# Optimization experiments

Measured on AMD Instinct MI355X. Metric: run time of the kernel, lower is better.

## Reference

```python
import jax, jax.numpy as jnp
import numpy as np
import math

B, S, H, NH, K = 1, 4096, 1024, 16, 32
HD = H // NH


def setup_inputs() -> dict:
    key = jax.random.key(0)
    ks = jax.random.split(key, 8)
    x = jax.random.normal(ks[0], (B, S, H), dtype=jnp.float32)
    # per-query top-K indices; make them causal (idx[q] <= q) so every row has >=1 valid key
    idx_raw = jax.random.randint(ks[1], (S, K), 0, S)
    idx = idx_raw % (jnp.arange(S)[:, None] + 1)
    valid = jnp.ones((S, K), dtype=bool)
    geo_bias = jax.random.normal(ks[2], (NH, S, K), dtype=jnp.float32)
    scale = 1.0 / math.sqrt(H)
    Wq = jax.random.normal(ks[3], (H, H), dtype=jnp.float32) * scale
    Wk = jax.random.normal(ks[4], (H, H), dtype=jnp.float32) * scale
    Wv = jax.random.normal(ks[5], (H, H), dtype=jnp.float32) * scale
    Wo = jax.random.normal(ks[6], (H, H), dtype=jnp.float32) * scale
    bo = jnp.zeros((H,), dtype=jnp.float32)
    return {"x": x, "idx": idx, "valid": valid, "geo_bias": geo_bias,
            "Wq": Wq, "Wk": Wk, "Wv": Wv, "Wo": Wo, "bo": bo}


def reference(x, idx, valid, geo_bias, Wq, Wk, Wv, Wo, bo):
    b, s, h = x.shape
    nh = geo_bias.shape[0]
    hd = h // nh
    kk = idx.shape[1]
    # projections -> [b, nh, s, hd]
    def proj(W):
        return (x @ W).reshape(b, s, nh, hd).transpose(0, 2, 1, 3)
    q, k, v = proj(Wq), proj(Wk), proj(Wv)
    # gather per-query selected keys/values: [b, nh, s, K, hd]
    k_sel = k[:, :, idx]
    v_sel = v[:, :, idx]
    # scores via elementwise mult + reduce over head_dim
    logits = jnp.einsum('bhsd,bhskd->bhsk', q, k_sel) / math.sqrt(hd)
    logits = logits + geo_bias[None]
    mask = valid & (idx <= jnp.arange(s)[:, None])  # [s, K]
    logits = jnp.where(mask[None, None], logits, jnp.float32(-1e30))
    attn = jax.nn.softmax(logits, axis=-1)
    out = jnp.einsum('bhsk,bhskd->bhsd', attn, v_sel)
    out = out.transpose(0, 2, 1, 3).reshape(b, s, h)
    return out @ Wo + bo
```

## Files before the change

kernel.cpp:

```cpp
#include <hip/hip_runtime.h>
#include <hip/hip_bf16.h>
#include <stdint.h>

typedef unsigned short u16;
typedef __attribute__((ext_vector_type(8))) short bf16x8;
typedef __attribute__((ext_vector_type(4))) float f32x4;
typedef __attribute__((ext_vector_type(2))) float f32x2;

typedef const __attribute__((address_space(1))) unsigned int* gptr_t;
typedef __attribute__((address_space(3))) unsigned int* lptr_t;

__device__ __forceinline__ u16 f2bf(float f) {
    unsigned int u;
    __builtin_memcpy(&u, &f, 4);
    u += 0x7FFFu + ((u >> 16) & 1u);
    return (u16)(u >> 16);
}
__device__ __forceinline__ float bflo(unsigned int u) {
    unsigned int x = u << 16; float f; __builtin_memcpy(&f, &x, 4); return f;
}
__device__ __forceinline__ float bfhi(unsigned int u) {
    unsigned int x = u & 0xFFFF0000u; float f; __builtin_memcpy(&f, &x, 4); return f;
}
__device__ __forceinline__ f32x2 upk(unsigned int u) {
    return (f32x2){bflo(u), bfhi(u)};
}

__global__ __launch_bounds__(256) void gemm_qkv(const u16* __restrict__ A,
                                                const u16* __restrict__ Bt,
                                                u16* __restrict__ C,
                                                int M, int N, int K) {
    __shared__ u16 S[4][4096];

    const int t    = threadIdx.x;
    const int lane = t & 63;
    const int wave = t >> 6;
    const int wm   = (wave >> 1) * 64;
    const int wn   = (wave & 1) * 64;
    const int m0   = blockIdx.y * 128;
    const int n0   = blockIdx.x * 128;

    const int r5   = t >> 2;
    const int pc   = t & 3;
    const int lc   = pc ^ ((r5 >> 1) & 3);

    const int quad = lane >> 4;
    const int l16  = lane & 15;
    const int swz  = (l16 >> 1) & 3;

    f32x4 acc[4][4];
#pragma unroll
    for (int i = 0; i < 4; i++)
#pragma unroll
        for (int j = 0; j < 4; j++) acc[i][j] = (f32x4){0.f, 0.f, 0.f, 0.f};

#pragma unroll
    for (int p = 0; p < 2; p++) {
        const u16* ga = A  + (size_t)(m0 + r5 + 64 * p) * K + lc * 8;
        const u16* gb = Bt + (size_t)(n0 + r5 + 64 * p) * K + lc * 8;
        __builtin_amdgcn_global_load_lds((gptr_t)ga, (lptr_t)(&S[0][t * 8 + p * 2048]), 16, 0, 0);
        __builtin_amdgcn_global_load_lds((gptr_t)gb, (lptr_t)(&S[2][t * 8 + p * 2048]), 16, 0, 0);
    }
    __syncthreads();

    const int NT = K >> 5;
    int cur = 0;
    for (int kt = 0; kt < NT; ++kt) {
        if (kt + 1 < NT) {
            const int k0 = (kt + 1) * 32;
#pragma unroll
            for (int p = 0; p < 2; p++) {
                const u16* ga = A  + (size_t)(m0 + r5 + 64 * p) * K + k0 + lc * 8;
                const u16* gb = Bt + (size_t)(n0 + r5 + 64 * p) * K + k0 + lc * 8;
                __builtin_amdgcn_global_load_lds((gptr_t)ga,
                    (lptr_t)(&S[cur ^ 1][t * 8 + p * 2048]), 16, 0, 0);
                __builtin_amdgcn_global_load_lds((gptr_t)gb,
                    (lptr_t)(&S[2 + (cur ^ 1)][t * 8 + p * 2048]), 16, 0, 0);
            }
        }

        bf16x8 af[4], bfg[4];
#pragma unroll
        for (int i = 0; i < 4; i++)
            af[i] = *(const bf16x8*)&S[cur][(wm + i * 16 + l16) * 32 + ((quad ^ swz) * 8)];
#pragma unroll
        for (int j = 0; j < 4; j++)
            bfg[j] = *(const bf16x8*)&S[2 + cur][(wn + j * 16 + l16) * 32 + ((quad ^ swz) * 8)];
#pragma unroll
        for (int i = 0; i < 4; i++)
#pragma unroll
            for (int j = 0; j < 4; j++)
                acc[i][j] = __builtin_amdgcn_mfma_f32_16x16x32_bf16(af[i], bfg[j], acc[i][j], 0, 0, 0);

        __syncthreads();
        cur ^= 1;
    }

    u16* Cs = &S[0][0];
#pragma unroll
    for (int j = 0; j < 4; j++)
#pragma unroll
        for (int i = 0; i < 4; i++)
#pragma unroll
            for (int r = 0; r < 4; r++)
                Cs[(wm + i * 16 + quad * 4 + r) * 128 + wn + j * 16 + l16] = f2bf(acc[i][j][r]);
    __syncthreads();

#pragma unroll
    for (int p = 0; p < 8; p++) {
        const int row = p * 16 + (t >> 4);
        const int c8  = (t & 15) * 8;
        const uint4 v = *(const uint4*)&Cs[row * 128 + c8];
        *(uint4*)&C[(size_t)(m0 + row) * N + n0 + c8] = v;
    }
}

__global__ __launch_bounds__(256) void gemm_o(const u16* __restrict__ A,
                                              const u16* __restrict__ Bt,
                                              float* __restrict__ C,
                                              const float* __restrict__ bias,
                                              int M, int N, int K) {
    __shared__ u16 As[128 * 64];
    __shared__ u16 Bs[64 * 64];

    const int t    = threadIdx.x;
    const int lane = t & 63;
    const int wave = t >> 6;
    const int wm   = (wave >> 1) * 64;
    const int wn   = (wave & 1) * 32;
    const int m0   = blockIdx.y * 128;
    const int n0   = blockIdx.x * 64;

    const int r5   = t >> 3;
    const int pc   = t & 7;
    const int lc   = pc ^ (r5 & 7);

    const int quad = lane >> 4;
    const int l16  = lane & 15;
    const int sw   = l16 & 7;

    f32x4 acc[4][2];
#pragma unroll
    for (int i = 0; i < 4; i++)
#pragma unroll
        for (int j = 0; j < 2; j++) acc[i][j] = (f32x4){0.f, 0.f, 0.f, 0.f};

    for (int k0 = 0; k0 < K; k0 += 64) {
#pragma unroll
        for (int p = 0; p < 4; p++) {
            const u16* ga = A + (size_t)(m0 + r5 + 32 * p) * K + k0 + lc * 8;
            __builtin_amdgcn_global_load_lds((gptr_t)ga, (lptr_t)(&As[t * 8 + p * 2048]), 16, 0, 0);
        }
#pragma unroll
        for (int p = 0; p < 2; p++) {
            const u16* gb = Bt + (size_t)(n0 + r5 + 32 * p) * K + k0 + lc * 8;
            __builtin_amdgcn_global_load_lds((gptr_t)gb, (lptr_t)(&Bs[t * 8 + p * 2048]), 16, 0, 0);
        }
        __syncthreads();

#pragma unroll
        for (int k2 = 0; k2 < 2; k2++) {
            bf16x8 af[4], bfg[2];
#pragma unroll
            for (int i = 0; i < 4; i++)
                af[i] = *(const bf16x8*)&As[(wm + i * 16 + l16) * 64 + ((k2 * 4 + quad) ^ sw) * 8];
#pragma unroll
            for (int j = 0; j < 2; j++)
                bfg[j] = *(const bf16x8*)&Bs[(wn + j * 16 + l16) * 64 + ((k2 * 4 + quad) ^ sw) * 8];
#pragma unroll
            for (int i = 0; i < 4; i++)
#pragma unroll
                for (int j = 0; j < 2; j++)
                    acc[i][j] = __builtin_amdgcn_mfma_f32_16x16x32_bf16(af[i], bfg[j], acc[i][j], 0, 0, 0);
        }
        __syncthreads();
    }

#pragma unroll
    for (int j = 0; j < 2; j++) {
        const int n  = n0 + wn + j * 16 + l16;
        const float bv = bias ? bias[n] : 0.f;
#pragma unroll
        for (int i = 0; i < 4; i++) {
            const int mbase = m0 + wm + i * 16 + quad * 4;
#pragma unroll
            for (int r = 0; r < 4; r++)
                C[(size_t)(mbase + r) * N + n] = acc[i][j][r] + bv;
        }
    }
}

__global__ __launch_bounds__(256) void prep_k(const float* __restrict__ x,
                                              const float* __restrict__ W0,
                                              const float* __restrict__ W1,
                                              const float* __restrict__ W2,
                                              const float* __restrict__ W3,
                                              u16* __restrict__ x_bf,
                                              u16* __restrict__ Dqkv,
                                              u16* __restrict__ Do) {
    const int b = blockIdx.x;
    if (b < 4096) {
        const int i = b * 256 + threadIdx.x;
        const float4 v = ((const float4*)x)[i];
        u16 o[4] = {f2bf(v.x), f2bf(v.y), f2bf(v.z), f2bf(v.w)};
        *(uint64_t*)&x_bf[i * 4] = *(uint64_t*)o;
        return;
    }
    __shared__ u16 tile[32][33];
    const int bb  = b - 4096;
    const int z   = bb >> 10;
    const int t10 = bb & 1023;
    const int c0  = (t10 & 31) * 32;
    const int r0  = (t10 >> 5) * 32;
    const float* src = (z == 0) ? W0 : (z == 1) ? W1 : (z == 2) ? W2 : W3;
    u16* dst = (z < 3) ? (Dqkv + (size_t)z * 1024 * 1024) : Do;
    const int tx = threadIdx.x & 31;
    const int ty = threadIdx.x >> 5;
#pragma unroll
    for (int i = 0; i < 32; i += 8)
        tile[ty + i][tx] = f2bf(src[(size_t)(r0 + ty + i) * 1024 + c0 + tx]);
    __syncthreads();
#pragma unroll
    for (int i = 0; i < 32; i += 8)
        dst[(size_t)(c0 + ty + i) * 1024 + r0 + tx] = tile[tx][ty + i];
}

__global__ __launch_bounds__(256, 6) void attn_k(const u16* __restrict__ QKV,
                                                 const int* __restrict__ idx,
                                                 const float* __restrict__ geo,
                                                 u16* __restrict__ AO) {
    __shared__ float dot_lds[4 * 64];
    __shared__ float w_lds[4 * 64];

    const int t    = threadIdx.x;
    const int lane = t & 63;
    const int wave = t >> 6;
    const int b    = blockIdx.x;
    const int hp   = b & 7;
    const int s    = ((b >> 3) << 2) + wave;
    const int h0   = hp * 2;
    const int hsel = lane >> 5;
    const int kk   = lane & 31;
    const int g    = lane >> 3;
    const int c8   = lane & 7;

    const char* qb = (const char*)QKV;

    const float gv = geo[((size_t)(h0 + hsel) * 4096 + s) * 32 + kk];
    const int j    = idx[s * 32 + kk];
    const int joff = j * 6144;

    const uint4 qA = *(const uint4*)(qb + (size_t)s * 6144 + h0 * 128 + c8 * 16);
    const uint4 qB = *(const uint4*)(qb + (size_t)s * 6144 + h0 * 128 + 128 + c8 * 16);

    int jsrc0 = __shfl(j, (0 * 8 + g) & 31);
    int jsrc1 = __shfl(j, (1 * 8 + g) & 31);
    int jsrc2 = __shfl(j, (2 * 8 + g) & 31);
    int jsrc3 = __shfl(j, (3 * 8 + g) & 31);

    uint4 kreg[8];
#pragma unroll
    for (int i = 0; i < 8; i++) {
        const int jm = (i & 3) == 0 ? jsrc0 : (i & 3) == 1 ? jsrc1
                     : (i & 3) == 2 ? jsrc2 : jsrc3;
        kreg[i] = *(const uint4*)(qb + (size_t)(unsigned)(jm * 6144) + 2048 +
                                  (h0 + (i >> 2)) * 128 + c8 * 16);
    }
    __builtin_amdgcn_sched_barrier(0);

    const f32x2 qa0 = upk(qA.x), qa1 = upk(qA.y), qa2 = upk(qA.z), qa3 = upk(qA.w);
    const f32x2 qb0 = upk(qB.x), qb1 = upk(qB.y), qb2 = upk(qB.z), qb3 = upk(qB.w);

#pragma unroll
    for (int i = 0; i < 8; i++) {
        const int rh = i * 8 + g;
        f32x2 d2;
        if (i < 4) {
            d2  = upk(kreg[i].x) * qa0;
            d2 += upk(kreg[i].y) * qa1;
            d2 += upk(kreg[i].z) * qa2;
            d2 += upk(kreg[i].w) * qa3;
        } else {
            d2  = upk(kreg[i].x) * qb0;
            d2 += upk(kreg[i].y) * qb1;
            d2 += upk(kreg[i].z) * qb2;
            d2 += upk(kreg[i].w) * qb3;
        }
        float d = d2.x + d2.y;
        d += __shfl_xor(d, 1);
        d += __shfl_xor(d, 2);
        d += __shfl_xor(d, 4);
        if (c8 == 0) dot_lds[wave * 64 + rh] = d;
    }

    float lg2 = dot_lds[wave * 64 + lane] * 0.125f + gv;
    if (j > s) lg2 = -1e30f;
    lg2 = fminf(lg2, 80.f);

    const float p = __expf(lg2);
    float sum = p;
    sum += __shfl_xor(sum, 16);
    sum += __shfl_xor(sum, 8);
    sum += __shfl_xor(sum, 4);
    sum += __shfl_xor(sum, 2);
    sum += __shfl_xor(sum, 1);
    const float w = p / sum;
    w_lds[wave * 64 + lane] = w;

    const int half = lane >> 5;
    const int e8   = lane & 31;
    const int vconst = 4096 + h0 * 128 + 8 * e8;
    uint2 vreg[16];
#pragma unroll
    for (int i = 0; i < 16; i++) {
        const int jo = __shfl(joff, 2 * i + half);
        vreg[i] = *(const uint2*)(qb + (size_t)(unsigned)jo + vconst);
    }
    __builtin_amdgcn_sched_barrier(0);

    const int whead = (e8 >> 4) * 32;
    f32x2 a01a = (f32x2){0.f, 0.f}, a01b = (f32x2){0.f, 0.f};
    f32x2 a23a = (f32x2){0.f, 0.f}, a23b = (f32x2){0.f, 0.f};
#pragma unroll
    for (int i = 0; i < 16; i += 2) {
        const float w0 = w_lds[wave * 64 + whead + 2 * i + half];
        const float w1 = w_lds[wave * 64 + whead + 2 * (i + 1) + half];
        a01a += w0 * upk(vreg[i].x);
        a23a += w0 * upk(vreg[i].y);
        a01b += w1 * upk(vreg[i + 1].x);
        a23b += w1 * upk(vreg[i + 1].y);
    }
    f32x2 av01 = a01a + a01b;
    f32x2 av23 = a23a + a23b;
    av01.x += __shfl_xor(av01.x, 32);
    av01.y += __shfl_xor(av01.y, 32);
    av23.x += __shfl_xor(av23.x, 32);
    av23.y += __shfl_xor(av23.y, 32);
    if (lane < 32) {
        u16 o[4] = {f2bf(av01.x), f2bf(av01.y), f2bf(av23.x), f2bf(av23.y)};
        *(uint2*)&AO[(size_t)s * 1024 + h0 * 64 + 4 * lane] = *(uint2*)o;
    }
}

extern "C" void kernel_launch(void* const* d_in, const int* in_sizes, int n_in,
                              void* d_out, int out_size, void* d_ws, size_t ws_size,
                              hipStream_t stream) {
    const float* x   = (const float*)d_in[0];
    const int*   idx = (const int*)d_in[1];
    const float* geo = (const float*)d_in[3];
    const float* Wq  = (const float*)d_in[4];
    const float* Wk  = (const float*)d_in[5];
    const float* Wv  = (const float*)d_in[6];
    const float* Wo  = (const float*)d_in[7];
    const float* bo  = (const float*)d_in[8];
    float* out = (float*)d_out;

    u16* x_bf   = (u16*)d_ws;
    u16* wt_qkv = x_bf + (size_t)4096 * 1024;
    u16* wt_o   = wt_qkv + (size_t)3 * 1024 * 1024;
    u16* qkv    = wt_o + (size_t)1024 * 1024;
    u16* ao     = qkv + (size_t)4096 * 3072;

    const dim3 tb(256);
    prep_k<<<dim3(8192), tb, 0, stream>>>(x, Wq, Wk, Wv, Wo, x_bf, wt_qkv, wt_o);

    gemm_qkv<<<dim3(3072 / 128, 4096 / 128), tb, 0, stream>>>(
        x_bf, wt_qkv, qkv, 4096, 3072, 1024);
    attn_k<<<dim3(4096 * 8 / 4), tb, 0, stream>>>(qkv, idx, geo, ao);
    gemm_o<<<dim3(1024 / 64, 4096 / 128), tb, 0, stream>>>(
        ao, wt_o, out, bo, 4096, 1024, 1024);
}
```

Measured before the change: 182.6 us.

## Deepen GEMM K-loop prefetch to two tiles with explicit vmcnt waits

```diff
diff --git a/kernel.cpp b/kernel.cpp
--- a/kernel.cpp
+++ b/kernel.cpp
@@ -48,53 +48,80 @@
     const int l16  = lane & 15;
     const int swz  = (l16 >> 1) & 3;
 
+    const u16* gabase = A  + (size_t)(m0 + r5) * K + lc * 8;
+    const u16* gbbase = Bt + (size_t)(n0 + r5) * K + lc * 8;
+
     f32x4 acc[4][4];
 #pragma unroll
     for (int i = 0; i < 4; i++)
 #pragma unroll
         for (int j = 0; j < 4; j++) acc[i][j] = (f32x4){0.f, 0.f, 0.f, 0.f};
 
+    const int NT = K >> 5;
+
 #pragma unroll
     for (int p = 0; p < 2; p++) {
-        const u16* ga = A  + (size_t)(m0 + r5 + 64 * p) * K + lc * 8;
-        const u16* gb = Bt + (size_t)(n0 + r5 + 64 * p) * K + lc * 8;
-        __builtin_amdgcn_global_load_lds((gptr_t)ga, (lptr_t)(&S[0][t * 8 + p * 2048]), 16, 0, 0);
-        __builtin_amdgcn_global_load_lds((gptr_t)gb, (lptr_t)(&S[2][t * 8 + p * 2048]), 16, 0, 0);
-    }
-    __syncthreads();
-
-    const int NT = K >> 5;
-    int cur = 0;
+        __builtin_amdgcn_global_load_lds((gptr_t)(gabase + (size_t)(64 * p) * K),
+                                         (lptr_t)(&S[0][t * 8 + p * 2048]), 16, 0, 0);
+        __builtin_amdgcn_global_load_lds((gptr_t)(gbbase + (size_t)(64 * p) * K),
+                                         (lptr_t)(&S[2][t * 8 + p * 2048]), 16, 0, 0);
+    }
+#pragma unroll
+    for (int p = 0; p < 2; p++) {
+        __builtin_amdgcn_global_load_lds((gptr_t)(gabase + (size_t)(64 * p) * K + 32),
+                                         (lptr_t)(&S[1][t * 8 + p * 2048]), 16, 0, 0);
+        __builtin_amdgcn_global_load_lds((gptr_t)(gbbase + (size_t)(64 * p) * K + 32),
+                                         (lptr_t)(&S[3][t * 8 + p * 2048]), 16, 0, 0);
+    }
+    asm volatile("s_waitcnt vmcnt(4)");
+    __builtin_amdgcn_sched_barrier(0);
+    __builtin_amdgcn_s_barrier();
+
     for (int kt = 0; kt < NT; ++kt) {
-        if (kt + 1 < NT) {
-            const int k0 = (kt + 1) * 32;
+        const int buf = kt & 1;
+
+        bf16x8 af[4], bfg[4];
+#pragma unroll
+        for (int i = 0; i < 4; i++)
+            af[i] = *(const bf16x8*)&S[buf][(wm + i * 16 + l16) * 32 + ((quad ^ swz) * 8)];
+#pragma unroll
+        for (int j = 0; j < 4; j++)
+            bfg[j] = *(const bf16x8*)&S[2 + buf][(wn + j * 16 + l16) * 32 + ((quad ^ swz) * 8)];
+        asm volatile("s_waitcnt lgkmcnt(0)");
+        __builtin_amdgcn_sched_barrier(0);
+        __builtin_amdgcn_s_barrier();
+
+        if (kt + 2 < NT) {
+            const int k0 = (kt + 2) * 32;
 #pragma unroll
             for (int p = 0; p < 2; p++) {
-                const u16* ga = A  + (size_t)(m0 + r5 + 64 * p) * K + k0 + lc * 8;
-                const u16* gb = Bt + (size_t)(n0 + r5 + 64 * p) * K + k0 + lc * 8;
-                __builtin_amdgcn_global_load_lds((gptr_t)ga,
-                    (lptr_t)(&S[cur ^ 1][t * 8 + p * 2048]), 16, 0, 0);
-                __builtin_amdgcn_global_load_lds((gptr_t)gb,
-                    (lptr_t)(&S[2 + (cur ^ 1)][t * 8 + p * 2048]), 16, 0, 0);
+                __builtin_amdgcn_global_load_lds(
+                    (gptr_t)(gabase + (size_t)(64 * p) * K + k0),
+                    (lptr_t)(&S[buf][t * 8 + p * 2048]), 16, 0, 0);
+                __builtin_amdgcn_global_load_lds(
+                    (gptr_t)(gbbase + (size_t)(64 * p) * K + k0),
+                    (lptr_t)(&S[2 + buf][t * 8 + p * 2048]), 16, 0, 0);
             }
         }
 
-        bf16x8 af[4], bfg[4];
-#pragma unroll
-        for (int i = 0; i < 4; i++)
-            af[i] = *(const bf16x8*)&S[cur][(wm + i * 16 + l16) * 32 + ((quad ^ swz) * 8)];
-#pragma unroll
-        for (int j = 0; j < 4; j++)
-            bfg[j] = *(const bf16x8*)&S[2 + cur][(wn + j * 16 + l16) * 32 + ((quad ^ swz) * 8)];
 #pragma unroll
         for (int i = 0; i < 4; i++)
 #pragma unroll
             for (int j = 0; j < 4; j++)
                 acc[i][j] = __builtin_amdgcn_mfma_f32_16x16x32_bf16(af[i], bfg[j], acc[i][j], 0, 0, 0);
 
-        __syncthreads();
-        cur ^= 1;
-    }
+        if (kt < NT - 2) {
+            asm volatile("s_waitcnt vmcnt(4)");
+            __builtin_amdgcn_sched_barrier(0);
+            __builtin_amdgcn_s_barrier();
+        } else if (kt == NT - 2) {
+            asm volatile("s_waitcnt vmcnt(0)");
+            __builtin_amdgcn_sched_barrier(0);
+            __builtin_amdgcn_s_barrier();
+        }
+    }
+
+    __syncthreads();
 
     u16* Cs = &S[0][0];
 #pragma unroll
```

Measured after the change: 182.0 us. About the same (-0.4%).
